# Kernel optimization log

Measured on AMD Instinct MI355X. Metric: run time of the kernel, lower is better.

Reference implementation:

```python
import jax, jax.numpy as jnp
import numpy as np

MASK_VALUE = -1e6


def setup_inputs() -> dict:
    key = jax.random.key(0)
    ks = jax.random.split(key, 8)
    B, Lq, Lk, D, H = 4, 512, 512, 128, 128
    return {
        "queries": jax.random.normal(ks[0], (B, Lq, D), dtype=jnp.float32),
        "keys": jax.random.normal(ks[1], (B, Lk, D), dtype=jnp.float32),
        "values": jax.random.normal(ks[2], (B, Lk, D), dtype=jnp.float32),
        "valid_seq_len": jax.random.randint(ks[3], (B,), 1, Lk + 1),
        "Wq": jax.random.normal(ks[4], (D, H), dtype=jnp.float32) * 0.05,
        "Wk": jax.random.normal(ks[5], (D, H), dtype=jnp.float32) * 0.05,
        "wv": jax.random.normal(ks[6], (H,), dtype=jnp.float32) * 0.05,
        "Wo": jax.random.normal(ks[7], (D, H), dtype=jnp.float32) * 0.05,
    }


def reference(queries, keys, values, valid_seq_len, Wq, Wk, wv, Wo):
    # q: (B,Lq,H), k: (B,Lk,H)
    q = jnp.einsum("bqd,dh->bqh", queries, Wq)
    k = jnp.einsum("bkd,dh->bkh", keys, Wk)
    # additive features: (B,Lq,Lk,H) -> scalar scores via wv
    feat = jnp.tanh(q[:, :, None, :] + k[:, None, :, :])
    scores = jnp.einsum("bqkh,h->bqk", feat, wv)
    # mask invalid key positions per batch (softmax over last dim)
    Lk = keys.shape[1]
    mask = jnp.arange(Lk)[None, None, :] < valid_seq_len[:, None, None]
    scores = jnp.where(mask, scores, MASK_VALUE)
    attn = jax.nn.softmax(scores, axis=-1)  # (B,Lq,Lk)
    out = jnp.einsum("bqk,bkd->bqd", attn, values)
    return jnp.einsum("bqd,dh->bqh", out, Wo)
```

## Files before the change

kernel.cpp:

```cpp
#include <hip/hip_runtime.h>
#include <hip/hip_bf16.h>

#define B_  4
#define LQ  512
#define LK  512
#define D_  128
#define H_  128
#define TQ  2

#define TWO_LOG2E 2.885390081777927f
#define LOG2E     1.442695040888963f

__device__ __forceinline__ float fexp2(float x) {
#if __has_builtin(__builtin_amdgcn_exp2f)
  return __builtin_amdgcn_exp2f(x);
#else
  return exp2f(x);
#endif
}
__device__ __forceinline__ float frcp(float x) {
#if __has_builtin(__builtin_amdgcn_rcpf)
  return __builtin_amdgcn_rcpf(x);
#else
  return __fdividef(1.0f, x);
#endif
}

__global__ __launch_bounds__(256) void proj_kernel(
    const float* __restrict__ queries, const float* __restrict__ keys,
    const float* __restrict__ Wq, const float* __restrict__ Wk,
    float* __restrict__ qproj, float* __restrict__ kproj) {
  __shared__ float s_x[8][D_];
  int r0 = blockIdx.x * 8;
  const float* X; const float* W; float* Y; int rb;
  if (r0 < B_ * LQ) { X = queries; W = Wq; Y = qproj; rb = r0; }
  else              { X = keys;    W = Wk; Y = kproj; rb = r0 - B_ * LQ; }
  int tid = threadIdx.x;
  for (int i = tid; i < 8 * D_; i += 256)
    s_x[i >> 7][i & 127] = X[(size_t)(rb + (i >> 7)) * D_ + (i & 127)];
  __syncthreads();
  int h = tid & 127, rh = tid >> 7;
  float a0 = 0.f, a1 = 0.f, a2 = 0.f, a3 = 0.f;
  #pragma unroll 8
  for (int d = 0; d < D_; ++d) {
    float w = W[d * H_ + h];
    a0 += s_x[rh * 4 + 0][d] * w;
    a1 += s_x[rh * 4 + 1][d] * w;
    a2 += s_x[rh * 4 + 2][d] * w;
    a3 += s_x[rh * 4 + 3][d] * w;
  }
  Y[(size_t)(rb + rh * 4 + 0) * H_ + h] = a0 * TWO_LOG2E;
  Y[(size_t)(rb + rh * 4 + 1) * H_ + h] = a1 * TWO_LOG2E;
  Y[(size_t)(rb + rh * 4 + 2) * H_ + h] = a2 * TWO_LOG2E;
  Y[(size_t)(rb + rh * 4 + 3) * H_ + h] = a3 * TWO_LOG2E;
}

__global__ __launch_bounds__(256) void attn_kernel(
    const float* __restrict__ qproj, const float* __restrict__ kproj,
    const float* __restrict__ values, const int* __restrict__ vlen_arr,
    const float* __restrict__ wv, const float* __restrict__ Wo,
    float* __restrict__ out) {
  int b  = blockIdx.y;
  int q0 = blockIdx.x * TQ;
  int tid = threadIdx.x;

  __shared__ float s_q[TQ][H_];
  __shared__ float s_wv[H_];
  __shared__ float s_sc[TQ][LK];
  __shared__ float s_po[2][TQ][D_];

  for (int i = tid; i < TQ * H_; i += 256)
    s_q[i >> 7][i & 127] = qproj[(size_t)(b * LQ + q0 + (i >> 7)) * H_ + (i & 127)];
  if (tid < H_) s_wv[tid] = wv[tid];
  __syncthreads();
  int vlen = vlen_arr[b];

  const float4* wv4p = (const float4*)s_wv;

  float sum_wv = 0.f;
  #pragma unroll
  for (int j = 0; j < H_ / 4; ++j) {
    float4 t = wv4p[j];
    sum_wv += t.x + t.y + t.z + t.w;
  }

  for (int kbase = 0; kbase < LK; kbase += 256) {
    int k = kbase + tid;
    if (k < vlen) {
      const float4* krow = (const float4*)(kproj + ((size_t)b * LK + k) * H_);
      float acc[TQ];
      #pragma unroll
      for (int ql = 0; ql < TQ; ++ql) acc[ql] = 0.f;
      #pragma unroll 8
      for (int h4 = 0; h4 < H_ / 4; ++h4) {
        float4 kv = krow[h4];
        float4 w4 = wv4p[h4];
        #pragma unroll
        for (int ql = 0; ql < TQ; ++ql) {
          float4 q4 = ((const float4*)s_q[ql])[h4];
          acc[ql] = fmaf(w4.x, frcp(fexp2(q4.x + kv.x) + 1.0f), acc[ql]);
          acc[ql] = fmaf(w4.y, frcp(fexp2(q4.y + kv.y) + 1.0f), acc[ql]);
          acc[ql] = fmaf(w4.z, frcp(fexp2(q4.z + kv.z) + 1.0f), acc[ql]);
          acc[ql] = fmaf(w4.w, frcp(fexp2(q4.w + kv.w) + 1.0f), acc[ql]);
        }
      }
      #pragma unroll
      for (int ql = 0; ql < TQ; ++ql)
        s_sc[ql][k] = fmaf(-2.0f, acc[ql], sum_wv);
    } else {
      #pragma unroll
      for (int ql = 0; ql < TQ; ++ql) s_sc[ql][k] = -1.0e6f;
    }
  }
  __syncthreads();

  int wave = tid >> 6, lane = tid & 63;

  if (wave < TQ) {
    float m = -3.0e38f;
    #pragma unroll
    for (int j = 0; j < LK / 64; ++j) m = fmaxf(m, s_sc[wave][lane + j * 64]);
    #pragma unroll
    for (int off = 32; off; off >>= 1) m = fmaxf(m, __shfl_xor(m, off));
    float sum = 0.f;
    float vals[LK / 64];
    #pragma unroll
    for (int j = 0; j < LK / 64; ++j) {
      float e = fexp2((s_sc[wave][lane + j * 64] - m) * LOG2E);
      vals[j] = e;
      sum += e;
    }
    #pragma unroll
    for (int off = 32; off; off >>= 1) sum += __shfl_xor(sum, off);
    float inv = frcp(sum);
    #pragma unroll
    for (int j = 0; j < LK / 64; ++j) s_sc[wave][lane + j * 64] = vals[j] * inv;
  }
  __syncthreads();

  {
    int row = wave >> 1, kc = wave & 1;
    int kend = min((((vlen + 3) >> 2) << 2), (kc + 1) * 256);
    const float2* vrow = (const float2*)(values + (size_t)b * LK * D_);
    float2 a = {0.f, 0.f};
    for (int k = kc * 256; k < kend; k += 4) {
      float4 sc4 = *((const float4*)&s_sc[row][k]);
      float2 v0 = vrow[(size_t)(k + 0) * 64 + lane];
      float2 v1 = vrow[(size_t)(k + 1) * 64 + lane];
      float2 v2 = vrow[(size_t)(k + 2) * 64 + lane];
      float2 v3 = vrow[(size_t)(k + 3) * 64 + lane];
      a.x += sc4.x * v0.x + sc4.y * v1.x + sc4.z * v2.x + sc4.w * v3.x;
      a.y += sc4.x * v0.y + sc4.y * v1.y + sc4.z * v2.y + sc4.w * v3.y;
    }
    s_po[kc][row][2 * lane]     = a.x;
    s_po[kc][row][2 * lane + 1] = a.y;
  }
  __syncthreads();

  {
    int ql = tid >> 7, h = tid & 127;
    float acc = 0.f;
    #pragma unroll 8
    for (int d = 0; d < D_; ++d)
      acc += (s_po[0][ql][d] + s_po[1][ql][d]) * Wo[d * H_ + h];
    out[((size_t)b * LQ + q0 + ql) * H_ + h] = acc;
  }
}

extern "C" void kernel_launch(void* const* d_in, const int* in_sizes, int n_in,
                              void* d_out, int out_size, void* d_ws, size_t ws_size,
                              hipStream_t stream) {
  const float* queries = (const float*)d_in[0];
  const float* keys    = (const float*)d_in[1];
  const float* values  = (const float*)d_in[2];
  const int*   vlen    = (const int*)d_in[3];
  const float* Wq      = (const float*)d_in[4];
  const float* Wk      = (const float*)d_in[5];
  const float* wv      = (const float*)d_in[6];
  const float* Wo      = (const float*)d_in[7];
  float* out = (float*)d_out;

  float* qproj = (float*)d_ws;
  float* kproj = qproj + (size_t)B_ * LQ * H_;

  proj_kernel<<<dim3(B_ * (LQ + LK) / 8), 256, 0, stream>>>(queries, keys, Wq, Wk, qproj, kproj);
  attn_kernel<<<dim3(LQ / TQ, B_), 256, 0, stream>>>(qproj, kproj, values, vlen, wv, Wo, out);
}
```

Measured before the change: 121.7 us.

## Transpose key projections and register-tile 2x2 query-key scores with larger blocks

The projection kernel now writes key projections transposed as (B,H,Lk), so that in the score loop adjacent threads load adjacent keys with coalesced float2 reads. Before, each thread read its own 512-byte key row. Each thread now computes a 2x2 tile of queries by keys, reusing every loaded key and query value twice. The attention block grows to 512 threads and 4 queries (TQ=4), which halves the number of blocks and the redundant value and Wo streaming per query. In exchange, register pressure rises and each block uses more shared memory, which may limit occupancy.

Measured after the change: 130.9 us. 7.6% more time.

```diff
diff --git a/kernel.cpp b/kernel.cpp
--- a/kernel.cpp
+++ b/kernel.cpp
@@ -6,7 +6,7 @@
 #define LK  512
 #define D_  128
 #define H_  128
-#define TQ  2
+#define TQ  4
 
 #define TWO_LOG2E 2.885390081777927f
 #define LOG2E     1.442695040888963f
@@ -29,12 +29,13 @@
 __global__ __launch_bounds__(256) void proj_kernel(
     const float* __restrict__ queries, const float* __restrict__ keys,
     const float* __restrict__ Wq, const float* __restrict__ Wk,
-    float* __restrict__ qproj, float* __restrict__ kproj) {
+    float* __restrict__ qproj, float* __restrict__ kT) {
   __shared__ float s_x[8][D_];
   int r0 = blockIdx.x * 8;
-  const float* X; const float* W; float* Y; int rb;
-  if (r0 < B_ * LQ) { X = queries; W = Wq; Y = qproj; rb = r0; }
-  else              { X = keys;    W = Wk; Y = kproj; rb = r0 - B_ * LQ; }
+  bool qside = r0 < B_ * LQ;
+  const float* X = qside ? queries : keys;
+  const float* W = qside ? Wq : Wk;
+  int rb = qside ? r0 : r0 - B_ * LQ;
   int tid = threadIdx.x;
   for (int i = tid; i < 8 * D_; i += 256)
     s_x[i >> 7][i & 127] = X[(size_t)(rb + (i >> 7)) * D_ + (i & 127)];
@@ -49,14 +50,23 @@
     a2 += s_x[rh * 4 + 2][d] * w;
     a3 += s_x[rh * 4 + 3][d] * w;
   }
-  Y[(size_t)(rb + rh * 4 + 0) * H_ + h] = a0 * TWO_LOG2E;
-  Y[(size_t)(rb + rh * 4 + 1) * H_ + h] = a1 * TWO_LOG2E;
-  Y[(size_t)(rb + rh * 4 + 2) * H_ + h] = a2 * TWO_LOG2E;
-  Y[(size_t)(rb + rh * 4 + 3) * H_ + h] = a3 * TWO_LOG2E;
-}
-
-__global__ __launch_bounds__(256) void attn_kernel(
-    const float* __restrict__ qproj, const float* __restrict__ kproj,
+  if (qside) {
+    qproj[(size_t)(rb + rh * 4 + 0) * H_ + h] = a0 * TWO_LOG2E;
+    qproj[(size_t)(rb + rh * 4 + 1) * H_ + h] = a1 * TWO_LOG2E;
+    qproj[(size_t)(rb + rh * 4 + 2) * H_ + h] = a2 * TWO_LOG2E;
+    qproj[(size_t)(rb + rh * 4 + 3) * H_ + h] = a3 * TWO_LOG2E;
+  } else {
+    int b = rb >> 9, kk = (rb & 511) + rh * 4;
+    float* dst = kT + ((size_t)b * H_ + h) * LK + kk;
+    dst[0] = a0 * TWO_LOG2E;
+    dst[1] = a1 * TWO_LOG2E;
+    dst[2] = a2 * TWO_LOG2E;
+    dst[3] = a3 * TWO_LOG2E;
+  }
+}
+
+__global__ __launch_bounds__(512, 4) void attn_kernel(
+    const float* __restrict__ qproj, const float* __restrict__ kT,
     const float* __restrict__ values, const int* __restrict__ vlen_arr,
     const float* __restrict__ wv, const float* __restrict__ Wo,
     float* __restrict__ out) {
@@ -69,14 +79,13 @@
   __shared__ float s_sc[TQ][LK];
   __shared__ float s_po[2][TQ][D_];
 
-  for (int i = tid; i < TQ * H_; i += 256)
+  for (int i = tid; i < TQ * H_; i += 512)
     s_q[i >> 7][i & 127] = qproj[(size_t)(b * LQ + q0 + (i >> 7)) * H_ + (i & 127)];
   if (tid < H_) s_wv[tid] = wv[tid];
   __syncthreads();
   int vlen = vlen_arr[b];
 
   const float4* wv4p = (const float4*)s_wv;
-
   float sum_wv = 0.f;
   #pragma unroll
   for (int j = 0; j < H_ / 4; ++j) {
@@ -84,32 +93,49 @@
     sum_wv += t.x + t.y + t.z + t.w;
   }
 
-  for (int kbase = 0; kbase < LK; kbase += 256) {
-    int k = kbase + tid;
+  {
+    int kt = tid & 255, qs = tid >> 8;
+    int k  = kt * 2;
     if (k < vlen) {
-      const float4* krow = (const float4*)(kproj + ((size_t)b * LK + k) * H_);
-      float acc[TQ];
-      #pragma unroll
-      for (int ql = 0; ql < TQ; ++ql) acc[ql] = 0.f;
-      #pragma unroll 8
+      const float2* kTp = (const float2*)(kT + (size_t)b * H_ * LK);
+      const float4* qap = (const float4*)s_q[qs * 2 + 0];
+      const float4* qbp = (const float4*)s_q[qs * 2 + 1];
+      float a00 = 0.f, a10 = 0.f, a01 = 0.f, a11 = 0.f;
+      #pragma unroll 4
       for (int h4 = 0; h4 < H_ / 4; ++h4) {
-        float4 kv = krow[h4];
+        float2 kv0 = kTp[(size_t)(4 * h4 + 0) * 256 + kt];
+        float2 kv1 = kTp[(size_t)(4 * h4 + 1) * 256 + kt];
+        float2 kv2 = kTp[(size_t)(4 * h4 + 2) * 256 + kt];
+        float2 kv3 = kTp[(size_t)(4 * h4 + 3) * 256 + kt];
         float4 w4 = wv4p[h4];
-        #pragma unroll
-        for (int ql = 0; ql < TQ; ++ql) {
-          float4 q4 = ((const float4*)s_q[ql])[h4];
-          acc[ql] = fmaf(w4.x, frcp(fexp2(q4.x + kv.x) + 1.0f), acc[ql]);
-          acc[ql] = fmaf(w4.y, frcp(fexp2(q4.y + kv.y) + 1.0f), acc[ql]);
-          acc[ql] = fmaf(w4.z, frcp(fexp2(q4.z + kv.z) + 1.0f), acc[ql]);
-          acc[ql] = fmaf(w4.w, frcp(fexp2(q4.w + kv.w) + 1.0f), acc[ql]);
-        }
+        float4 qa = qap[h4];
+        float4 qb = qbp[h4];
+        a00 = fmaf(w4.x, frcp(fexp2(qa.x + kv0.x) + 1.f), a00);
+        a10 = fmaf(w4.x, frcp(fexp2(qa.x + kv0.y) + 1.f), a10);
+        a01 = fmaf(w4.x, frcp(fexp2(qb.x + kv0.x) + 1.f), a01);
+        a11 = fmaf(w4.x, frcp(fexp2(qb.x + kv0.y) + 1.f), a11);
+        a00 = fmaf(w4.y, frcp(fexp2(qa.y + kv1.x) + 1.f), a00);
+        a10 = fmaf(w4.y, frcp(fexp2(qa.y + kv1.y) + 1.f), a10);
+        a01 = fmaf(w4.y, frcp(fexp2(qb.y + kv1.x) + 1.f), a01);
+        a11 = fmaf(w4.y, frcp(fexp2(qb.y + kv1.y) + 1.f), a11);
+        a00 = fmaf(w4.z, frcp(fexp2(qa.z + kv2.x) + 1.f), a00);
+        a10 = fmaf(w4.z, frcp(fexp2(qa.z + kv2.y) + 1.f), a10);
+        a01 = fmaf(w4.z, frcp(fexp2(qb.z + kv2.x) + 1.f), a01);
+        a11 = fmaf(w4.z, frcp(fexp2(qb.z + kv2.y) + 1.f), a11);
+        a00 = fmaf(w4.w, frcp(fexp2(qa.w + kv3.x) + 1.f), a00);
+        a10 = fmaf(w4.w, frcp(fexp2(qa.w + kv3.y) + 1.f), a10);
+        a01 = fmaf(w4.w, frcp(fexp2(qb.w + kv3.x) + 1.f), a01);
+        a11 = fmaf(w4.w, frcp(fexp2(qb.w + kv3.y) + 1.f), a11);
       }
-      #pragma unroll
-      for (int ql = 0; ql < TQ; ++ql)
-        s_sc[ql][k] = fmaf(-2.0f, acc[ql], sum_wv);
+      bool m1 = (k + 1) < vlen;
+      float2 r0 = { fmaf(-2.f, a00, sum_wv), m1 ? fmaf(-2.f, a10, sum_wv) : -1.0e6f };
+      float2 r1 = { fmaf(-2.f, a01, sum_wv), m1 ? fmaf(-2.f, a11, sum_wv) : -1.0e6f };
+      ((float2*)s_sc[qs * 2 + 0])[kt] = r0;
+      ((float2*)s_sc[qs * 2 + 1])[kt] = r1;
     } else {
-      #pragma unroll
-      for (int ql = 0; ql < TQ; ++ql) s_sc[ql][k] = -1.0e6f;
+      float2 mm = { -1.0e6f, -1.0e6f };
+      ((float2*)s_sc[qs * 2 + 0])[kt] = mm;
+      ((float2*)s_sc[qs * 2 + 1])[kt] = mm;
     }
   }
   __syncthreads();
@@ -181,8 +207,8 @@
   float* out = (float*)d_out;
 
   float* qproj = (float*)d_ws;
-  float* kproj = qproj + (size_t)B_ * LQ * H_;
-
-  proj_kernel<<<dim3(B_ * (LQ + LK) / 8), 256, 0, stream>>>(queries, keys, Wq, Wk, qproj, kproj);
-  attn_kernel<<<dim3(LQ / TQ, B_), 256, 0, stream>>>(qproj, kproj, values, vlen, wv, Wo, out);
-}
+  float* kT    = qproj + (size_t)B_ * LQ * H_;
+
+  proj_kernel<<<dim3(B_ * (LQ + LK) / 8), 256, 0, stream>>>(queries, keys, Wq, Wk, qproj, kT);
+  attn_kernel<<<dim3(LQ / TQ, B_), 512, 0, stream>>>(qproj, kT, values, vlen, wv, Wo, out);
+}
```
